# Performance work log

Measured on AMD Instinct MI355X. Metric: run time of the kernel, lower is better.

The kernel has to match this reference:

```python
import jax, jax.numpy as jnp
import numpy as np

BN_EPS = 1e-5


def _binary_activation(x):
    # forward value = sign(x); gradient flows through piecewise poly o3 (STE)
    s = jnp.sign(x)
    o1 = jnp.where(x < -1.0, -1.0, x * x + 2.0 * x)
    o2 = jnp.where(x < 0.0, o1, -x * x + 2.0 * x)
    o3 = jnp.where(x < 1.0, o2, 1.0)
    return jax.lax.stop_gradient(s - o3) + o3


def _binarize_weights(w):
    # sign_function: fwd 2*(w>0)-1, bwd identity (STE)
    sgn = 2.0 * (w > 0.0).astype(w.dtype) - 1.0
    wb = jax.lax.stop_gradient(sgn - w) + w
    # detached per-output-channel scale: mean |w| over (in, kh, kw)
    scale = jax.lax.stop_gradient(jnp.mean(jnp.abs(w), axis=(1, 2, 3), keepdims=True))
    return scale * wb


def setup_inputs() -> dict:
    key = jax.random.key(0)
    k1, k2, k3 = jax.random.split(key, 3)
    C = 64
    x = jax.random.normal(k1, (32, C, 112, 112), dtype=jnp.float32)
    w = jax.random.uniform(k2, (C, C, 3, 3), dtype=jnp.float32) * 0.001
    return {
        "x": x,
        "b0": jnp.zeros((1, C, 1, 1), jnp.float32),
        "w": w,
        "gamma": jnp.ones((C,), jnp.float32),
        "beta": jnp.zeros((C,), jnp.float32),
        "b1": jnp.zeros((1, C, 1, 1), jnp.float32),
        "alpha": jnp.full((C,), 0.25, jnp.float32),  # PReLU default init
        "b2": jnp.zeros((1, C, 1, 1), jnp.float32),
    }


def reference(x, b0, w, gamma, beta, b1, alpha, b2):
    residual = x
    out = x + b0                       # move0
    out = _binary_activation(out)      # binary activation
    bw = _binarize_weights(w)
    out = jax.lax.conv_general_dilated(
        out, bw, window_strides=(1, 1), padding=[(1, 1), (1, 1)],
        dimension_numbers=("NCHW", "OIHW", "NCHW"))
    # BatchNorm2d in training mode (batch stats, biased variance)
    mu = jnp.mean(out, axis=(0, 2, 3), keepdims=True)
    var = jnp.var(out, axis=(0, 2, 3), keepdims=True)
    g = gamma.reshape(1, -1, 1, 1)
    b = beta.reshape(1, -1, 1, 1)
    out = (out - mu) * jax.lax.rsqrt(var + BN_EPS) * g + b
    out = out + residual
    out = out + b1                     # move1
    a = alpha.reshape(1, -1, 1, 1)
    out = jnp.where(out > 0, out, a * out)  # PReLU
    out = out + b2                     # move2
    return out
```

## Files before the change

### kernel.cpp

```cpp
#include <hip/hip_runtime.h>
#include <stdint.h>

#define C 64
#define HH 112
#define WWD 112
#define HW (HH*WWD)
#define NB 32
#define MTOT (NB*HW)
#define PPR 56
#define PPI 6272
#define PACK_BLKS 1568
#define OH 32

__global__ __launch_bounds__(256) void k_prep_pack(
        const float* __restrict__ x, const float* __restrict__ b0,
        const float* __restrict__ w,
        uint64_t* __restrict__ xp,
        uint64_t* __restrict__ wbits, float* __restrict__ wscale,
        int* __restrict__ corrP) {
    int bid = blockIdx.x;
    if (bid < PACK_BLKS) {
        int n = bid / 49;
        int pix = (bid % 49) * 256 + threadIdx.x;
        uint64_t p = 0;
        const float* xb = x + (size_t)n * C * HW + pix;
        #pragma unroll
        for (int c = 0; c < C; ++c) {
            float v = xb[(size_t)c * HW] + b0[c];
            p |= (uint64_t)(v > 0.f) << c;
        }
        xp[(size_t)n*HW + pix] = p;
    } else {
        if (threadIdx.x >= 64) return;
        int o = bid - PACK_BLKS;
        int i = threadIdx.x;
        const float* wp = w + ((size_t)o*C + i)*9;
        float s = 0.f;
        uint64_t b[9];
        #pragma unroll
        for (int k = 0; k < 9; ++k) {
            float v = wp[k];
            s += fabsf(v);
            b[k] = __ballot(v > 0.f);
        }
        #pragma unroll
        for (int off = 32; off > 0; off >>= 1) s += __shfl_down(s, off);
        if (i == 0) {
            wscale[o] = s * (1.0f/576.0f);
            int pq[9];
            #pragma unroll
            for (int k = 0; k < 9; ++k) {
                wbits[o*9+k] = b[k];
                pq[k] = __popcll(b[k]);
            }
            for (int rc = 0; rc < 3; ++rc)
                for (int cc = 0; cc < 3; ++cc) {
                    int corr = 0;
                    for (int kr = 0; kr < 3; ++kr)
                        for (int kc = 0; kc < 3; ++kc) {
                            bool oob = (rc==0 && kr==0) || (rc==2 && kr==2) ||
                                       (cc==0 && kc==0) || (cc==2 && kc==2);
                            if (oob) corr += 64 - 2*pq[kr*3+kc];
                        }
                    corrP[(rc*3+cc)*C + o] = 576 - corr;
                }
        }
    }
}

__global__ __launch_bounds__(256) void k_conv(
        const uint64_t* __restrict__ xp, const uint64_t* __restrict__ wbits,
        const int* __restrict__ corrP, uint32_t* __restrict__ cv) {
    __shared__ uint64_t sq[OH*9];
    __shared__ int scor[9*OH];
    const int obase = blockIdx.z * OH;
    for (int i = threadIdx.x; i < OH*9; i += 256) sq[i] = wbits[obase*9 + i];
    for (int i = threadIdx.x; i < 9*OH; i += 256) {
        int r = i / OH, oo = i - r*OH;
        scor[i] = corrP[r*C + obase + oo];
    }
    __syncthreads();
    int n = blockIdx.y;
    int pr = blockIdx.x * 256 + threadIdx.x;
    if (pr >= PPI) return;
    int row = pr / PPR;
    int j   = pr - row * PPR;
    int c0  = 2 * j;
    const uint64_t* base = xp + (size_t)n * HW;
    uint64_t P[12];
    #pragma unroll
    for (int r = 0; r < 3; ++r) {
        int rr = row + r - 1;
        bool okr = (rr >= 0) & (rr < HH);
        #pragma unroll
        for (int c = 0; c < 4; ++c) {
            int cc = c0 + c - 1;
            bool ok = okr & (cc >= 0) & (cc < WWD);
            P[r*4+c] = ok ? base[(size_t)rr * WWD + cc] : 0ull;
        }
    }
    int rc  = (row == 0) ? 0 : ((row == HH-1) ? 2 : 1);
    int reg0 = (rc*3 + ((c0 == 0) ? 0 : 1)) * OH;
    int reg1 = (rc*3 + ((c0 == WWD-2) ? 2 : 1)) * OH;
    uint32_t* op = cv + ((size_t)n * C + obase) * HW + pr;
    for (int oo = 0; oo < OH; ++oo) {
        const uint64_t* q = &sq[oo*9];
        int a0 = 0, a1 = 0;
        #pragma unroll
        for (int r = 0; r < 3; ++r) {
            #pragma unroll
            for (int c = 0; c < 3; ++c) {
                uint64_t qk = q[r*3+c];
                a0 += __popcll(P[r*4+c]   ^ qk);
                a1 += __popcll(P[r*4+c+1] ^ qk);
            }
        }
        int v0 = scor[reg0 + oo] - 2*a0;
        int v1 = scor[reg1 + oo] - 2*a1;
        op[0] = (uint32_t)(uint16_t)v0 | ((uint32_t)(uint16_t)v1 << 16);
        op += HW;
    }
}

__global__ __launch_bounds__(256) void k_stats(
        const uint32_t* __restrict__ cv, float* __restrict__ psum,
        float* __restrict__ psumsq) {
    int o = blockIdx.x & 63;
    int n = blockIdx.x >> 6;
    const uint32_t* p = cv + ((size_t)n * C + o) * HW;
    float s = 0.f, s2 = 0.f;
    for (int i = threadIdx.x; i < PPI/2; i += 256) {
        uint2 u = ((const uint2*)p)[i];
        float v0 = (float)(int)(short)(u.x & 0xFFFF);
        float v1 = (float)(int)(short)(u.x >> 16);
        float v2 = (float)(int)(short)(u.y & 0xFFFF);
        float v3 = (float)(int)(short)(u.y >> 16);
        s  += (v0 + v1) + (v2 + v3);
        s2 += (v0*v0 + v1*v1) + (v2*v2 + v3*v3);
    }
    __shared__ float ls[256], ls2[256];
    ls[threadIdx.x] = s; ls2[threadIdx.x] = s2;
    __syncthreads();
    for (int st = 128; st > 0; st >>= 1) {
        if ((int)threadIdx.x < st) {
            ls[threadIdx.x]  += ls[threadIdx.x+st];
            ls2[threadIdx.x] += ls2[threadIdx.x+st];
        }
        __syncthreads();
    }
    if (threadIdx.x == 0) { psum[o*NB + n] = ls[0]; psumsq[o*NB + n] = ls2[0]; }
}

__global__ __launch_bounds__(256) void k_finish(
        const uint32_t* cvi, const float* __restrict__ x,
        const float* __restrict__ psum, const float* __restrict__ psumsq,
        const float* __restrict__ wscale, const float* __restrict__ gamma,
        const float* __restrict__ beta, const float* __restrict__ b1,
        const float* __restrict__ alpha, const float* __restrict__ b2,
        float* out) {
    int o = blockIdx.x & 63;
    int n = blockIdx.x >> 6;
    size_t plane = (size_t)n * C + o;

    __shared__ uint32_t sk[PPI];
    const uint32_t* kp = cvi + plane * HW;
    for (int i = threadIdx.x; i < PPI; i += 256) sk[i] = kp[i];

    float s = 0.f, s2 = 0.f;
    #pragma unroll 8
    for (int t = 0; t < NB; ++t) { s += psum[o*NB+t]; s2 += psumsq[o*NB+t]; }
    const float inv = 1.0f / (float)MTOT;
    float sc  = wscale[o];
    float mu  = sc * (s * inv);
    float ek2 = (sc * sc) * (s2 * inv);
    float var = ek2 - mu * mu;
    float g   = gamma[o] * rsqrtf(var + 1e-5f);
    float A   = g * sc;
    float B   = beta[o] - g * mu + b1[o];
    float al  = alpha[o];
    float bb2 = b2[o];

    __syncthreads();

    const float4* xp4 = (const float4*)(x + plane * HW);
    float4* op = (float4*)(out + plane * HW);
    for (int i = threadIdx.x; i < HW/4; i += 256) {
        uint2 u = *(const uint2*)&sk[2*i];
        float4 xv = xp4[i], r;
        float t;
        t = A * (float)(int)(short)(u.x & 0xFFFF) + B + xv.x; t = t > 0.f ? t : al*t; r.x = t + bb2;
        t = A * (float)(int)(short)(u.x >> 16)    + B + xv.y; t = t > 0.f ? t : al*t; r.y = t + bb2;
        t = A * (float)(int)(short)(u.y & 0xFFFF) + B + xv.z; t = t > 0.f ? t : al*t; r.z = t + bb2;
        t = A * (float)(int)(short)(u.y >> 16)    + B + xv.w; t = t > 0.f ? t : al*t; r.w = t + bb2;
        op[i] = r;
    }
}

extern "C" void kernel_launch(void* const* d_in, const int* in_sizes, int n_in,
                              void* d_out, int out_size, void* d_ws, size_t ws_size,
                              hipStream_t stream) {
    const float* x     = (const float*)d_in[0];
    const float* b0    = (const float*)d_in[1];
    const float* w     = (const float*)d_in[2];
    const float* gamma = (const float*)d_in[3];
    const float* beta  = (const float*)d_in[4];
    const float* b1    = (const float*)d_in[5];
    const float* alpha = (const float*)d_in[6];
    const float* b2    = (const float*)d_in[7];

    char* ws = (char*)d_ws;
    const size_t XPB = (size_t)NB * HW * sizeof(uint64_t);
    uint64_t* xp     = (uint64_t*)ws;
    uint64_t* wbits  = (uint64_t*)(ws + XPB);
    float*    wscale = (float*)(ws + XPB + C*9*sizeof(uint64_t));
    int*      corrP  = (int*)(wscale + C);
    float*    psum   = (float*)(corrP + 9*C);
    float*    psumsq = psum + C*NB;

    uint32_t* cv = (uint32_t*)d_out;

    hipLaunchKernelGGL(k_prep_pack, dim3(PACK_BLKS + 64), dim3(256), 0, stream,
                       x, b0, w, xp, wbits, wscale, corrP);
    hipLaunchKernelGGL(k_conv, dim3((PPI + 255)/256, NB, 2), dim3(256), 0, stream,
                       xp, wbits, corrP, cv);
    hipLaunchKernelGGL(k_stats, dim3(C*NB), dim3(256), 0, stream, cv, psum, psumsq);
    hipLaunchKernelGGL(k_finish, dim3(C*NB), dim3(256), 0, stream,
                       cv, x, psum, psumsq, wscale, gamma, beta, b1, alpha, b2,
                       (float*)d_out);
}
```

Before: 113.6 us.

## Recompute binary conv in finish pass instead of storing intermediate conv output

Replaces the conv-store, stats-read and finish-read pipeline with two passes over the packed bits. The first pass computes the XNOR-popcount conv and reduces per-channel sum and sum of squares in integers, using wave shuffles and atomics into 8 slots per channel. The second pass recomputes the conv, applies BN, residual and PReLU, and writes the output directly. This removes the 16-bit intermediate round trip through global memory and the separate stats kernel, at the cost of doing the popcount conv twice and relying on the prep kernel to zero the atomic accumulators.

```diff
diff --git a/kernel.cpp b/kernel.cpp
--- a/kernel.cpp
+++ b/kernel.cpp
@@ -10,14 +10,16 @@
 #define PPR 56
 #define PPI 6272
 #define PACK_BLKS 1568
-#define OH 32
+#define CONV_BLKS 25
+
+typedef unsigned long long u64t;
 
 __global__ __launch_bounds__(256) void k_prep_pack(
         const float* __restrict__ x, const float* __restrict__ b0,
         const float* __restrict__ w,
         uint64_t* __restrict__ xp,
         uint64_t* __restrict__ wbits, float* __restrict__ wscale,
-        int* __restrict__ corrP) {
+        int* __restrict__ corrP, int* __restrict__ ps, u64t* __restrict__ pq) {
     int bid = blockIdx.x;
     if (bid < PACK_BLKS) {
         int n = bid / 49;
@@ -31,55 +33,149 @@
         }
         xp[(size_t)n*HW + pix] = p;
     } else {
-        if (threadIdx.x >= 64) return;
+        int tid = threadIdx.x;
         int o = bid - PACK_BLKS;
-        int i = threadIdx.x;
-        const float* wp = w + ((size_t)o*C + i)*9;
-        float s = 0.f;
-        uint64_t b[9];
-        #pragma unroll
-        for (int k = 0; k < 9; ++k) {
-            float v = wp[k];
-            s += fabsf(v);
-            b[k] = __ballot(v > 0.f);
-        }
-        #pragma unroll
-        for (int off = 32; off > 0; off >>= 1) s += __shfl_down(s, off);
-        if (i == 0) {
-            wscale[o] = s * (1.0f/576.0f);
-            int pq[9];
+        if (tid < 64) {
+            int i = tid;
+            const float* wp = w + ((size_t)o*C + i)*9;
+            float s = 0.f;
+            uint64_t b[9];
             #pragma unroll
             for (int k = 0; k < 9; ++k) {
-                wbits[o*9+k] = b[k];
-                pq[k] = __popcll(b[k]);
-            }
-            for (int rc = 0; rc < 3; ++rc)
-                for (int cc = 0; cc < 3; ++cc) {
-                    int corr = 0;
-                    for (int kr = 0; kr < 3; ++kr)
-                        for (int kc = 0; kc < 3; ++kc) {
-                            bool oob = (rc==0 && kr==0) || (rc==2 && kr==2) ||
-                                       (cc==0 && kc==0) || (cc==2 && kc==2);
-                            if (oob) corr += 64 - 2*pq[kr*3+kc];
-                        }
-                    corrP[(rc*3+cc)*C + o] = 576 - corr;
+                float v = wp[k];
+                s += fabsf(v);
+                b[k] = __ballot(v > 0.f);
+            }
+            #pragma unroll
+            for (int off = 32; off > 0; off >>= 1) s += __shfl_down(s, off);
+            if (i == 0) {
+                wscale[o] = s * (1.0f/576.0f);
+                int pq9[9];
+                #pragma unroll
+                for (int k = 0; k < 9; ++k) {
+                    wbits[o*9+k] = b[k];
+                    pq9[k] = __popcll(b[k]);
                 }
-        }
-    }
-}
-
-__global__ __launch_bounds__(256) void k_conv(
+                for (int rc = 0; rc < 3; ++rc)
+                    for (int cc = 0; cc < 3; ++cc) {
+                        int corr = 0;
+                        for (int kr = 0; kr < 3; ++kr)
+                            for (int kc = 0; kc < 3; ++kc) {
+                                bool oob = (rc==0 && kr==0) || (rc==2 && kr==2) ||
+                                           (cc==0 && kc==0) || (cc==2 && kc==2);
+                                if (oob) corr += 64 - 2*pq9[kr*3+kc];
+                            }
+                        corrP[(rc*3+cc)*C + o] = 576 - corr;
+                    }
+            }
+        } else if (bid == PACK_BLKS) {
+            for (int i = tid - 64; i < C*8; i += 192) { ps[i] = 0; pq[i] = 0ull; }
+        }
+    }
+}
+
+__global__ __launch_bounds__(256) void k_convstats(
         const uint64_t* __restrict__ xp, const uint64_t* __restrict__ wbits,
-        const int* __restrict__ corrP, uint32_t* __restrict__ cv) {
-    __shared__ uint64_t sq[OH*9];
-    __shared__ int scor[9*OH];
-    const int obase = blockIdx.z * OH;
-    for (int i = threadIdx.x; i < OH*9; i += 256) sq[i] = wbits[obase*9 + i];
-    for (int i = threadIdx.x; i < 9*OH; i += 256) {
-        int r = i / OH, oo = i - r*OH;
-        scor[i] = corrP[r*C + obase + oo];
-    }
+        const int* __restrict__ corrP, int* __restrict__ ps, u64t* __restrict__ pq) {
+    __shared__ uint64_t sq[C*9];
+    __shared__ int scor[9*C];
+    __shared__ int lsw[4][C];
+    __shared__ int lqw[4][C];
+    for (int i = threadIdx.x; i < C*9; i += 256) sq[i] = wbits[i];
+    for (int i = threadIdx.x; i < 9*C; i += 256) scor[i] = corrP[i];
     __syncthreads();
+
+    int n = blockIdx.y;
+    int pr = blockIdx.x * 256 + threadIdx.x;
+    int act = pr < PPI;
+    int prc = act ? pr : (PPI - 1);
+    int row = prc / PPR;
+    int j   = prc - row * PPR;
+    int c0  = 2 * j;
+    const uint64_t* base = xp + (size_t)n * HW;
+    uint64_t P[12];
+    #pragma unroll
+    for (int r = 0; r < 3; ++r) {
+        int rr = row + r - 1;
+        bool okr = (rr >= 0) & (rr < HH);
+        #pragma unroll
+        for (int c = 0; c < 4; ++c) {
+            int cc = c0 + c - 1;
+            bool ok = okr & (cc >= 0) & (cc < WWD);
+            P[r*4+c] = ok ? base[(size_t)rr * WWD + cc] : 0ull;
+        }
+    }
+    int rc   = (row == 0) ? 0 : ((row == HH-1) ? 2 : 1);
+    int reg0 = (rc*3 + ((c0 == 0) ? 0 : 1)) * C;
+    int reg1 = (rc*3 + ((c0 == WWD-2) ? 2 : 1)) * C;
+    int wid = threadIdx.x >> 6, lane = threadIdx.x & 63;
+
+    #pragma unroll 2
+    for (int o = 0; o < C; ++o) {
+        const uint64_t* q = &sq[o*9];
+        int a0 = 0, a1 = 0;
+        #pragma unroll
+        for (int r = 0; r < 3; ++r) {
+            #pragma unroll
+            for (int c = 0; c < 3; ++c) {
+                uint64_t qk = q[r*3+c];
+                a0 += __popcll(P[r*4+c]   ^ qk);
+                a1 += __popcll(P[r*4+c+1] ^ qk);
+            }
+        }
+        int v0 = scor[reg0 + o] - 2*a0;
+        int v1 = scor[reg1 + o] - 2*a1;
+        int s = act ? (v0 + v1) : 0;
+        int qq = act ? (v0*v0 + v1*v1) : 0;
+        #pragma unroll
+        for (int off = 1; off < 64; off <<= 1) {
+            s  += __shfl_xor(s,  off);
+            qq += __shfl_xor(qq, off);
+        }
+        if (lane == 0) { lsw[wid][o] = s; lqw[wid][o] = qq; }
+    }
+    __syncthreads();
+    int t = threadIdx.x;
+    if (t < C) {
+        int st = lsw[0][t] + lsw[1][t] + lsw[2][t] + lsw[3][t];
+        atomicAdd(&ps[t*8 + (n & 7)], st);
+    } else if (t < 2*C) {
+        int o = t - C;
+        unsigned int qt = (unsigned)lqw[0][o] + (unsigned)lqw[1][o]
+                        + (unsigned)lqw[2][o] + (unsigned)lqw[3][o];
+        atomicAdd(&pq[o*8 + (n & 7)], (u64t)qt);
+    }
+}
+
+__global__ __launch_bounds__(256) void k_finish(
+        const uint64_t* __restrict__ xp, const uint64_t* __restrict__ wbits,
+        const int* __restrict__ corrP, const int* __restrict__ ps,
+        const u64t* __restrict__ pq, const float* __restrict__ x,
+        const float* __restrict__ wscale, const float* __restrict__ gamma,
+        const float* __restrict__ beta, const float* __restrict__ b1,
+        const float* __restrict__ alpha, const float* __restrict__ b2,
+        float* __restrict__ out) {
+    __shared__ uint64_t sq[C*9];
+    __shared__ int scor[9*C];
+    __shared__ float4 tab[C];
+    for (int i = threadIdx.x; i < C*9; i += 256) sq[i] = wbits[i];
+    for (int i = threadIdx.x; i < 9*C; i += 256) scor[i] = corrP[i];
+    if (threadIdx.x < C) {
+        int o = threadIdx.x;
+        int s = 0; u64t qv = 0;
+        #pragma unroll
+        for (int k = 0; k < 8; ++k) { s += ps[o*8+k]; qv += pq[o*8+k]; }
+        const float inv = 1.0f / (float)MTOT;
+        float sc   = wscale[o];
+        float mean = (float)s * inv;
+        float ek2  = (float)qv * inv;
+        float mu   = sc * mean;
+        float var  = sc*sc*ek2 - mu*mu;
+        float g    = gamma[o] * rsqrtf(var + 1e-5f);
+        tab[o] = make_float4(g*sc, beta[o] - g*mu + b1[o], alpha[o], b2[o]);
+    }
+    __syncthreads();
+
     int n = blockIdx.y;
     int pr = blockIdx.x * 256 + threadIdx.x;
     if (pr >= PPI) return;
@@ -99,12 +195,14 @@
             P[r*4+c] = ok ? base[(size_t)rr * WWD + cc] : 0ull;
         }
     }
-    int rc  = (row == 0) ? 0 : ((row == HH-1) ? 2 : 1);
-    int reg0 = (rc*3 + ((c0 == 0) ? 0 : 1)) * OH;
-    int reg1 = (rc*3 + ((c0 == WWD-2) ? 2 : 1)) * OH;
-    uint32_t* op = cv + ((size_t)n * C + obase) * HW + pr;
-    for (int oo = 0; oo < OH; ++oo) {
-        const uint64_t* q = &sq[oo*9];
+    int rc   = (row == 0) ? 0 : ((row == HH-1) ? 2 : 1);
+    int reg0 = (rc*3 + ((c0 == 0) ? 0 : 1)) * C;
+    int reg1 = (rc*3 + ((c0 == WWD-2) ? 2 : 1)) * C;
+
+    const float2* x2 = (const float2*)x + (size_t)n * C * (HW/2) + pr;
+    float2*       o2 = (float2*)out     + (size_t)n * C * (HW/2) + pr;
+    for (int o = 0; o < C; ++o) {
+        const uint64_t* q = &sq[o*9];
         int a0 = 0, a1 = 0;
         #pragma unroll
         for (int r = 0; r < 3; ++r) {
@@ -115,84 +213,15 @@
                 a1 += __popcll(P[r*4+c+1] ^ qk);
             }
         }
-        int v0 = scor[reg0 + oo] - 2*a0;
-        int v1 = scor[reg1 + oo] - 2*a1;
-        op[0] = (uint32_t)(uint16_t)v0 | ((uint32_t)(uint16_t)v1 << 16);
-        op += HW;
-    }
-}
-
-__global__ __launch_bounds__(256) void k_stats(
-        const uint32_t* __restrict__ cv, float* __restrict__ psum,
-        float* __restrict__ psumsq) {
-    int o = blockIdx.x & 63;
-    int n = blockIdx.x >> 6;
-    const uint32_t* p = cv + ((size_t)n * C + o) * HW;
-    float s = 0.f, s2 = 0.f;
-    for (int i = threadIdx.x; i < PPI/2; i += 256) {
-        uint2 u = ((const uint2*)p)[i];
-        float v0 = (float)(int)(short)(u.x & 0xFFFF);
-        float v1 = (float)(int)(short)(u.x >> 16);
-        float v2 = (float)(int)(short)(u.y & 0xFFFF);
-        float v3 = (float)(int)(short)(u.y >> 16);
-        s  += (v0 + v1) + (v2 + v3);
-        s2 += (v0*v0 + v1*v1) + (v2*v2 + v3*v3);
-    }
-    __shared__ float ls[256], ls2[256];
-    ls[threadIdx.x] = s; ls2[threadIdx.x] = s2;
-    __syncthreads();
-    for (int st = 128; st > 0; st >>= 1) {
-        if ((int)threadIdx.x < st) {
-            ls[threadIdx.x]  += ls[threadIdx.x+st];
-            ls2[threadIdx.x] += ls2[threadIdx.x+st];
-        }
-        __syncthreads();
-    }
-    if (threadIdx.x == 0) { psum[o*NB + n] = ls[0]; psumsq[o*NB + n] = ls2[0]; }
-}
-
-__global__ __launch_bounds__(256) void k_finish(
-        const uint32_t* cvi, const float* __restrict__ x,
-        const float* __restrict__ psum, const float* __restrict__ psumsq,
-        const float* __restrict__ wscale, const float* __restrict__ gamma,
-        const float* __restrict__ beta, const float* __restrict__ b1,
-        const float* __restrict__ alpha, const float* __restrict__ b2,
-        float* out) {
-    int o = blockIdx.x & 63;
-    int n = blockIdx.x >> 6;
-    size_t plane = (size_t)n * C + o;
-
-    __shared__ uint32_t sk[PPI];
-    const uint32_t* kp = cvi + plane * HW;
-    for (int i = threadIdx.x; i < PPI; i += 256) sk[i] = kp[i];
-
-    float s = 0.f, s2 = 0.f;
-    #pragma unroll 8
-    for (int t = 0; t < NB; ++t) { s += psum[o*NB+t]; s2 += psumsq[o*NB+t]; }
-    const float inv = 1.0f / (float)MTOT;
-    float sc  = wscale[o];
-    float mu  = sc * (s * inv);
-    float ek2 = (sc * sc) * (s2 * inv);
-    float var = ek2 - mu * mu;
-    float g   = gamma[o] * rsqrtf(var + 1e-5f);
-    float A   = g * sc;
-    float B   = beta[o] - g * mu + b1[o];
-    float al  = alpha[o];
-    float bb2 = b2[o];
-
-    __syncthreads();
-
-    const float4* xp4 = (const float4*)(x + plane * HW);
-    float4* op = (float4*)(out + plane * HW);
-    for (int i = threadIdx.x; i < HW/4; i += 256) {
-        uint2 u = *(const uint2*)&sk[2*i];
-        float4 xv = xp4[i], r;
-        float t;
-        t = A * (float)(int)(short)(u.x & 0xFFFF) + B + xv.x; t = t > 0.f ? t : al*t; r.x = t + bb2;
-        t = A * (float)(int)(short)(u.x >> 16)    + B + xv.y; t = t > 0.f ? t : al*t; r.y = t + bb2;
-        t = A * (float)(int)(short)(u.y & 0xFFFF) + B + xv.z; t = t > 0.f ? t : al*t; r.z = t + bb2;
-        t = A * (float)(int)(short)(u.y >> 16)    + B + xv.w; t = t > 0.f ? t : al*t; r.w = t + bb2;
-        op[i] = r;
+        int v0 = scor[reg0 + o] - 2*a0;
+        int v1 = scor[reg1 + o] - 2*a1;
+        float4 t4 = tab[o];
+        float2 xv = x2[(size_t)o * (HW/2)];
+        float t0 = t4.x * (float)v0 + t4.y + xv.x;
+        float t1 = t4.x * (float)v1 + t4.y + xv.y;
+        t0 = t0 > 0.f ? t0 : t4.z * t0;
+        t1 = t1 > 0.f ? t1 : t4.z * t1;
+        o2[(size_t)o * (HW/2)] = make_float2(t0 + t4.w, t1 + t4.w);
     }
 }
 
@@ -212,19 +241,16 @@
     const size_t XPB = (size_t)NB * HW * sizeof(uint64_t);
     uint64_t* xp     = (uint64_t*)ws;
     uint64_t* wbits  = (uint64_t*)(ws + XPB);
-    float*    wscale = (float*)(ws + XPB + C*9*sizeof(uint64_t));
-    int*      corrP  = (int*)(wscale + C);
-    float*    psum   = (float*)(corrP + 9*C);
-    float*    psumsq = psum + C*NB;
-
-    uint32_t* cv = (uint32_t*)d_out;
+    u64t*     pq     = (u64t*)(ws + XPB + 4608);
+    float*    wscale = (float*)(ws + XPB + 4608 + 4096);
+    int*      corrP  = (int*)(ws + XPB + 4608 + 4096 + 256);
+    int*      ps     = (int*)(ws + XPB + 4608 + 4096 + 256 + 2304);
 
     hipLaunchKernelGGL(k_prep_pack, dim3(PACK_BLKS + 64), dim3(256), 0, stream,
-                       x, b0, w, xp, wbits, wscale, corrP);
-    hipLaunchKernelGGL(k_conv, dim3((PPI + 255)/256, NB, 2), dim3(256), 0, stream,
-                       xp, wbits, corrP, cv);
-    hipLaunchKernelGGL(k_stats, dim3(C*NB), dim3(256), 0, stream, cv, psum, psumsq);
-    hipLaunchKernelGGL(k_finish, dim3(C*NB), dim3(256), 0, stream,
-                       cv, x, psum, psumsq, wscale, gamma, beta, b1, alpha, b2,
+                       x, b0, w, xp, wbits, wscale, corrP, ps, pq);
+    hipLaunchKernelGGL(k_convstats, dim3(CONV_BLKS, NB), dim3(256), 0, stream,
+                       xp, wbits, corrP, ps, pq);
+    hipLaunchKernelGGL(k_finish, dim3(CONV_BLKS, NB), dim3(256), 0, stream,
+                       xp, wbits, corrP, ps, pq, x, wscale, gamma, beta, b1, alpha, b2,
                        (float*)d_out);
 }
```

Result: slower. 150.4 us (+32.4%).
